# Kernel optimization log

Hardware: AMD Instinct MI355X
Metric: run time of the kernel (lower is better)

## Reference

```python
import jax, jax.numpy as jnp
import numpy as np

MIN_DIST = 4
BASE_PRIMES = np.array([2, 3, 5, 7])  # A, C, G, U
# canonical pair prime products: AU=2*7=14, CG=3*5=15, GU=5*7=35


def nussinov(s):
    """Nussinov max-score non-crossing pairing: O(N^3) DP (vectorized per
    anti-diagonal) + stack-based traceback. s: [N,N] float64, symmetric, >=0.
    Returns symmetric 0/1 pair mask. Mirrors kirigami.nussinov (CPU numpy)."""
    N = s.shape[0]
    D = np.zeros((N, N))  # D[d, i] = dp[i, i+d]
    E = np.zeros((N, N))  # E[d, j] = dp[j-d, j]
    ar = np.arange(N)
    for d in range(1, N):
        m = N - d
        pair = (D[d - 2, 1:m + 1] if d >= 2 else 0.0) + s[ar[:m], ar[:m] + d]
        # split over k=i..j-1: dp[i,k] + dp[k+1,j] (k=i covers i-unpaired)
        split = (D[0:d, 0:m] + E[d - 1::-1, d:N]).max(axis=0)
        val = np.maximum(pair, split)
        D[d, :m] = val
        E[d, d:] = val
    dp = np.zeros((N, N))
    for d in range(1, N):
        dp[ar[:N - d], ar[:N - d] + d] = D[d, :N - d]
    eps = 1e-9
    pm = np.zeros((N, N))
    stack = [(0, N - 1)]
    while stack:
        i, j = stack.pop()
        if j <= i:
            continue
        v = dp[i, j]
        if v <= eps:
            continue
        if dp[i + 1, j] >= v - eps:
            stack.append((i + 1, j))
        elif s[i, j] > 0 and dp[i + 1, j - 1] + s[i, j] >= v - eps:
            pm[i, j] = pm[j, i] = 1.0
            stack.append((i + 1, j - 1))
        else:
            ks = np.arange(i, j)
            k = int(ks[np.argmax(dp[i, ks] + dp[ks + 1, j])])
            stack.append((i, k))
            stack.append((k + 1, j))
    return pm


def _premask(con, feat):
    """Symmetrize + remove sharp angles (tril(-4)+triu(4)) + canonical-pair mask."""
    c = con[0, 0]                      # [N, N]
    c = (c + c.T) * 0.5                # Symmetrize
    N = c.shape[0]
    idx = jnp.arange(N)
    dist_ok = jnp.abs(idx[:, None] - idx[None, :]) >= MIN_DIST  # RemoveSharp
    seq = feat[0, :4, :, 0]            # [4, N] one-hot base encoding
    primes = jnp.asarray(BASE_PRIMES)[jnp.argmax(seq, axis=0)]  # [N]
    prod = primes[:, None] * primes[None, :]
    canon = (prod == 14) | (prod == 15) | (prod == 35)          # Canonicalize
    return c * (dist_ok & canon)


def setup_inputs() -> dict:
    key = jax.random.key(0)
    k1, k2 = jax.random.split(key)
    N = 1024
    con = jax.random.uniform(k1, (1, 1, N, N), dtype=jnp.float32)
    feat = jax.random.normal(k2, (1, 16, N, N), dtype=jnp.float32)
    return {"con": con, "feat": feat}


def reference(con, feat):
    c = _premask(con, feat)
    # original: GPU->CPU numpy float64 DP, then mask back on device
    mask = nussinov(np.asarray(c, dtype=np.float64))
    out = c * jnp.asarray(mask, dtype=c.dtype)
    return out.reshape(con.shape)
```

## Files before the change

### kernel.cpp

```cpp
#include <hip/hip_runtime.h>

#define NN 1024
#define BT 32
#define TT 32
#define NTILES ((TT * (TT + 1)) / 2)

__device__ __forceinline__ double gload_cc(const double* p) {
    double v;
    asm volatile("global_load_dwordx2 %0, %1, off sc0 sc1" : "=v"(v) : "v"(p));
    return v;
}
__device__ __forceinline__ void gstore_cc(double* p, double v) {
    asm volatile("global_store_dwordx2 %0, %1, off sc0 sc1" :: "v"(p), "v"(v));
}
__device__ __forceinline__ void gstore_flag(int* p, int v) {
    asm volatile("global_store_dword %0, %1, off sc0 sc1" :: "v"(p), "v"(v));
}
#define VWAIT0 asm volatile("s_waitcnt vmcnt(0)" ::: "memory")

__device__ __forceinline__ void waitflag2(const int* f, int a0, int b0, int a1, int b1) {
    const int* p0 = &f[(a0 * TT + b0) << 4];
    const int* p1 = &f[(a1 * TT + b1) << 4];
    int it = 0;
    while (true) {
        int v0, v1;
        asm volatile("global_load_dword %0, %2, off sc0 sc1\n\t"
                     "global_load_dword %1, %3, off sc0 sc1\n\t"
                     "s_waitcnt vmcnt(0)"
                     : "=&v"(v0), "=&v"(v1)
                     : "v"(p0), "v"(p1));
        if (v0 & v1) break;
        if (it < 8) __builtin_amdgcn_s_sleep(1);
        else        __builtin_amdgcn_s_sleep(15);
        ++it;
    }
    asm volatile("" ::: "memory");
}
__device__ __forceinline__ void waitflag4(const int* f, int a0, int b0, int a1, int b1,
                                          int a2, int b2, int a3, int b3) {
    const int* p0 = &f[(a0 * TT + b0) << 4];
    const int* p1 = &f[(a1 * TT + b1) << 4];
    const int* p2 = &f[(a2 * TT + b2) << 4];
    const int* p3 = &f[(a3 * TT + b3) << 4];
    int it = 0;
    while (true) {
        int v0, v1, v2, v3;
        asm volatile("global_load_dword %0, %4, off sc0 sc1\n\t"
                     "global_load_dword %1, %5, off sc0 sc1\n\t"
                     "global_load_dword %2, %6, off sc0 sc1\n\t"
                     "global_load_dword %3, %7, off sc0 sc1\n\t"
                     "s_waitcnt vmcnt(0)"
                     : "=&v"(v0), "=&v"(v1), "=&v"(v2), "=&v"(v3)
                     : "v"(p0), "v"(p1), "v"(p2), "v"(p3));
        if (v0 & v1 & v2 & v3) break;
        if (it < 8) __builtin_amdgcn_s_sleep(1);
        else        __builtin_amdgcn_s_sleep(15);
        ++it;
    }
    asm volatile("" ::: "memory");
}
__device__ __forceinline__ void waitflag2_blk(const int* f, int a0, int b0, int a1, int b1) {
    if (threadIdx.x < 64) waitflag2(f, a0, b0, a1, b1);
    __syncthreads();
}
__device__ __forceinline__ void waitflag4_blk(const int* f, int a0, int b0, int a1, int b1,
                                              int a2, int b2, int a3, int b3) {
    if (threadIdx.x < 64) waitflag4(f, a0, b0, a1, b1, a2, b2, a3, b3);
    __syncthreads();
}

__global__ void primes_kernel(const float* __restrict__ feat, int* __restrict__ primes) {
    int i = blockIdx.x * blockDim.x + threadIdx.x;
    if (i < NN) {
        float best = feat[i * NN];
        int arg = 0;
        for (int ch = 1; ch < 4; ++ch) {
            float v = feat[ch * NN * NN + i * NN];
            if (v > best) { best = v; arg = ch; }
        }
        const int P[4] = {2, 3, 5, 7};
        primes[i] = P[arg];
    }
}

__global__ void prep_kernel(const float* __restrict__ con, const int* __restrict__ primes,
                            float* __restrict__ S, double* __restrict__ R,
                            double* __restrict__ C, float* __restrict__ out,
                            int* __restrict__ flags,
                            int* __restrict__ qi, int* __restrict__ qj,
                            int* __restrict__ qready, int* __restrict__ qctl) {
    int idx = blockIdx.x * blockDim.x + threadIdx.x;
    int i = idx >> 10;
    int j = idx & (NN - 1);
    float c = (con[idx] + con[j * NN + i]) * 0.5f;
    int prod = primes[i] * primes[j];
    bool canon = (prod == 14) | (prod == 15) | (prod == 35);
    int d = i - j; if (d < 0) d = -d;
    S[idx] = (canon && d >= 4) ? c : 0.0f;
    R[idx] = 0.0;
    C[idx] = 0.0;
    out[idx] = 0.0f;
    if (idx < TT * TT * 16) flags[idx] = 0;
    if (idx < 4096) qready[idx] = (idx == 0) ? 1 : 0;
    if (idx == 0) {
        qi[0] = 0; qj[0] = NN - 1;
        qctl[0] = 0;
        qctl[16] = 1;
        qctl[32] = 1;
    }
}

__global__ __launch_bounds__(256) void nuss_tiles_kernel(double* __restrict__ R,
                                                         double* __restrict__ C,
                                                         const float* __restrict__ S,
                                                         int* __restrict__ flags) {
    __shared__ double DJJc[32][33];
    __shared__ double Vtc[32][33];
    __shared__ __attribute__((aligned(16))) double Ast[32][34];
    __shared__ __attribute__((aligned(16))) double Bst[32][34];
    __shared__ double Pld[32][33];
    __shared__ float  Sld[32][32];
    __shared__ double edgeCol[33];
    __shared__ __attribute__((aligned(16))) double Prt[3][32][6];

    int b = blockIdx.x, dd = 0;
    while (b >= TT - dd) { b -= TT - dd; ++dd; }
    const int I = b, J = b + dd;
    const int aI = I * BT, aJ = J * BT;
    const int tid = threadIdx.x;
    const int wid = tid >> 6;
    const int lane = tid & 63;
    const int r = lane >> 1;
    const int h = lane & 1;

    if (dd == 0) {
        #pragma unroll
        for (int w = 0; w < 4; ++w) {
            int idx = w * 256 + tid; int rr = idx >> 5, cc = idx & 31;
            Sld[rr][cc] = S[(aI + rr) * NN + aI + cc];
        }
        for (int idx = tid; idx < 32 * 33; idx += 256)
            ((double*)Vtc)[idx] = 0.0;
        __syncthreads();
        if (wid == 0) {
            double vrow[16];
            #pragma unroll
            for (int u = 0; u < 16; ++u) vrow[u] = 0.0;
            for (int s = 1; s <= 31; ++s) {
                int c = r + s;
                bool act = (c <= 31);
                double acc = 0.0;
                if (act) {
                    double t0 = 0.0, t1 = 0.0, t2 = 0.0, t3 = 0.0;
                    #pragma unroll
                    for (int u = 0; u < 16; u += 4) {
                        int k0 = h * 16 + u;
                        t0 = fmax(t0, vrow[u]     + Vtc[c][k0 + 1]);
                        t1 = fmax(t1, vrow[u + 1] + Vtc[c][k0 + 2]);
                        t2 = fmax(t2, vrow[u + 2] + Vtc[c][k0 + 3]);
                        t3 = fmax(t3, vrow[u + 3] + Vtc[c][k0 + 4]);
                    }
                    acc = fmax(fmax(t0, t1), fmax(t2, t3));
                }
                acc = fmax(acc, __shfl_xor(acc, 1));
                if (act) {
                    double best = fmax(acc, Vtc[c - 1][r + 1] + (double)Sld[r][c]);
                    if (h == 0) Vtc[c][r] = best;
                    #pragma unroll
                    for (int u = 0; u < 16; ++u)
                        if (h * 16 + u == c) vrow[u] = best;
                }
            }
        }
        __syncthreads();
        #pragma unroll
        for (int w = 0; w < 4; ++w) {
            int idx = w * 256 + tid; int rr = idx >> 5, cc = idx & 31;
            gstore_cc(&R[(aI + rr) * NN + aI + cc], Vtc[cc][rr]);
        }
        #pragma unroll
        for (int w = 0; w < 4; ++w) {
            int idx = w * 256 + tid; int cc = idx >> 5, rr = idx & 31;
            gstore_cc(&C[(aI + cc) * NN + aI + rr], Vtc[cc][rr]);
        }
        VWAIT0;
        __syncthreads();
        if (tid == 0) gstore_flag(&flags[(I * TT + I) << 4], 1);
        return;
    }

    const int nk = dd - 1;
    const int off = (wid & 1) * 16 + h * 8;
    waitflag2_blk(flags, I, I, J, J);

    double ra[4], rb[4];
    double ec = 0.0, ve = 0.0;
    double asl[8];
    double ar1 = 0.0;
    #pragma unroll
    for (int w = 0; w < 4; ++w) {
        int idx = w * 256 + tid; int cc = idx >> 5, mm = idx & 31;
        ra[w] = gload_cc(&C[(aJ + cc) * NN + aJ + mm]);
    }
    if (wid < 2) {
        #pragma unroll
        for (int u = 0; u < 8; ++u)
            asl[u] = gload_cc(&R[(aI + r) * NN + aI + off + u]);
    }
    if (r < 31) ar1 = gload_cc(&R[(aI + r) * NN + aI + r + 1]);
    if (wid == 0 && nk == 0) {
        if (lane < 33) ec = gload_cc(&R[(aI + lane) * NN + (aJ - 1)]);
        if (lane < 32) ve = gload_cc(&R[(aI + 32) * NN + aJ + lane]);
    }
    #pragma unroll
    for (int w = 0; w < 4; ++w) {
        int idx = w * 256 + tid; int rr = idx >> 5, cc = idx & 31;
        Sld[rr][cc] = S[(aI + rr) * NN + aJ + cc];
    }
    for (int idx = tid; idx < 32 * 33; idx += 256)
        ((double*)Vtc)[idx] = 0.0;
    VWAIT0;
    #pragma unroll
    for (int w = 0; w < 4; ++w) {
        int idx = w * 256 + tid; int cc = idx >> 5, mm = idx & 31;
        DJJc[cc][mm] = ra[w];
    }
    if (tid < 32) DJJc[tid][32] = 0.0;
    double slice8[8];
    if (wid < 2) {
        #pragma unroll
        for (int u = 0; u < 8; ++u)
            slice8[u] = (off + u > r + 1) ? asl[u] : -1.0e30;
    } else {
        #pragma unroll
        for (int u = 0; u < 8; ++u) slice8[u] = 0.0;
    }
    if (wid == 0 && nk == 0) {
        if (lane < 33) edgeCol[lane] = ec;
        if (lane < 32) Vtc[lane][32] = ve;
    }
    __syncthreads();

    double P[16];
    #pragma unroll
    for (int x = 0; x < 16; ++x) P[x] = 0.0;
    const int rg = lane >> 3, cg = lane & 7;
    const int r4 = rg * 4, c4 = cg * 4;

    auto kkloop = [&]() {
        for (int kk = wid * 8; kk < wid * 8 + 8; ++kk) {
            double2 av0 = *(const double2*)&Ast[kk][r4];
            double2 av1 = *(const double2*)&Ast[kk][r4 + 2];
            double2 bv0 = *(const double2*)&Bst[kk][c4];
            double2 bv1 = *(const double2*)&Bst[kk][c4 + 2];
            P[0]  = fmax(P[0],  av0.x + bv0.x); P[1]  = fmax(P[1],  av0.x + bv0.y);
            P[2]  = fmax(P[2],  av0.x + bv1.x); P[3]  = fmax(P[3],  av0.x + bv1.y);
            P[4]  = fmax(P[4],  av0.y + bv0.x); P[5]  = fmax(P[5],  av0.y + bv0.y);
            P[6]  = fmax(P[6],  av0.y + bv1.x); P[7]  = fmax(P[7],  av0.y + bv1.y);
            P[8]  = fmax(P[8],  av1.x + bv0.x); P[9]  = fmax(P[9],  av1.x + bv0.y);
            P[10] = fmax(P[10], av1.x + bv1.x); P[11] = fmax(P[11], av1.x + bv1.y);
            P[12] = fmax(P[12], av1.y + bv0.x); P[13] = fmax(P[13], av1.y + bv0.y);
            P[14] = fmax(P[14], av1.y + bv1.x); P[15] = fmax(P[15], av1.y + bv1.y);
        }
    };
    auto proc = [&](int t1, int t2, bool last) {
        if (t2 >= 0) waitflag4_blk(flags, I, t1, t1, J, I, t2, t2, J);
        else         waitflag2_blk(flags, I, t1, t1, J);
        if (last && wid == 0) {
            if (lane < 33) ec = gload_cc(&R[(aI + lane) * NN + (aJ - 1)]);
            if (lane < 32) ve = gload_cc(&R[(aI + 32) * NN + aJ + lane]);
        }
        int k1 = t1 * BT;
        #pragma unroll
        for (int w = 0; w < 4; ++w) {
            int idx = w * 256 + tid; int rr = idx >> 5, kk = idx & 31;
            ra[w] = gload_cc(&R[(aI + rr) * NN + k1 + kk]);
            rb[w] = gload_cc(&C[(aJ + rr) * NN + k1 + 1 + kk]);
        }
        VWAIT0;
        #pragma unroll
        for (int w = 0; w < 4; ++w) {
            int idx = w * 256 + tid; int rr = idx >> 5, kk = idx & 31;
            Ast[kk][rr] = ra[w];
            Bst[kk][rr] = rb[w];
        }
        if (last && wid == 0) {
            if (lane < 33) edgeCol[lane] = ec;
            if (lane < 32) Vtc[lane][32] = ve;
        }
        __syncthreads();
        if (t2 >= 0) {
            int k2 = t2 * BT;
            #pragma unroll
            for (int w = 0; w < 4; ++w) {
                int idx = w * 256 + tid; int rr = idx >> 5, kk = idx & 31;
                ra[w] = gload_cc(&R[(aI + rr) * NN + k2 + kk]);
                rb[w] = gload_cc(&C[(aJ + rr) * NN + k2 + 1 + kk]);
            }
        }
        kkloop();
        if (t2 >= 0) {
            __syncthreads();
            VWAIT0;
            #pragma unroll
            for (int w = 0; w < 4; ++w) {
                int idx = w * 256 + tid; int rr = idx >> 5, kk = idx & 31;
                Ast[kk][rr] = ra[w];
                Bst[kk][rr] = rb[w];
            }
            __syncthreads();
            kkloop();
        }
        __syncthreads();
    };

    {
        int tl = (I + J) >> 1, tr = ((I + J) >> 1) + 1;
        int pend = -1;
        for (int q = 0; q < nk; ++q) {
            int t;
            if ((q & 1) == 0) { if (tl >= I + 1) t = tl--; else t = tr++; }
            else              { if (tr <= J - 1) t = tr++; else t = tl--; }
            if (pend < 0) { pend = t; continue; }
            int rp = (pend - I > J - pend) ? pend - I : J - pend;
            int rt = (t - I > J - t) ? t - I : J - t;
            if (rp == rt) { proc(pend, t, q == nk - 1); pend = -1; }
            else          { proc(pend, -1, false); pend = t; }
        }
        if (pend >= 0) proc(pend, -1, true);
    }

    if (nk > 0) {
        if (wid == 0) {
            #pragma unroll
            for (int x = 0; x < 4; ++x)
                #pragma unroll
                for (int y = 0; y < 4; ++y)
                    Pld[r4 + x][c4 + y] = P[x * 4 + y];
        }
        __syncthreads();
        if (wid == 1) {
            #pragma unroll
            for (int x = 0; x < 4; ++x)
                #pragma unroll
                for (int y = 0; y < 4; ++y)
                    Pld[r4 + x][c4 + y] = fmax(Pld[r4 + x][c4 + y], P[x * 4 + y]);
        }
        __syncthreads();
        if (wid == 2) {
            #pragma unroll
            for (int x = 0; x < 4; ++x)
                #pragma unroll
                for (int y = 0; y < 4; ++y)
                    Pld[r4 + x][c4 + y] = fmax(Pld[r4 + x][c4 + y], P[x * 4 + y]);
        }
        __syncthreads();
        if (wid == 3) {
            #pragma unroll
            for (int x = 0; x < 4; ++x)
                #pragma unroll
                for (int y = 0; y < 4; ++y)
                    Pld[r4 + x][c4 + y] = fmax(Pld[r4 + x][c4 + y], P[x * 4 + y]);
        }
        __syncthreads();
    } else {
        for (int idx = tid; idx < 32 * 33; idx += 256)
            ((double*)Pld)[idx] = 0.0;
        __syncthreads();
    }

    {
        const double* bsel = (wid < 2) ? &Vtc[0][0] : &DJJc[0][0];
        double ecr = edgeCol[r];
        double ecp = edgeCol[r + 1];
        double pv[8];
        double p1 = 0.0, p2 = 0.0, shc = 0.0, shp = 0.0, erc = 0.0, erp = 0.0;

#define PREFQ(SS)                                                     \
    { int cq_ = (r + (SS) - 31) & 31;                                 \
      const double* bp_ = bsel + cq_ * 33 + off + 1;                  \
      _Pragma("unroll")                                               \
      for (int u = 0; u < 8; ++u) pv[u] = bp_[u]; }

#define PARTQ(SS)                                                     \
    { double t0_ = fmax(slice8[0] + pv[0], slice8[1] + pv[1]);        \
      double t1_ = fmax(slice8[2] + pv[2], slice8[3] + pv[3]);        \
      double t2_ = fmax(slice8[4] + pv[4], slice8[5] + pv[5]);        \
      double t3_ = fmax(slice8[6] + pv[6], slice8[7] + pv[7]);        \
      double pa_ = fmax(fmax(t0_, t1_), fmax(t2_, t3_));              \
      pa_ = fmax(pa_, __shfl_xor(pa_, 1));                            \
      if (h == 0) Prt[(SS) % 3][r][wid] = pa_; }

#define STEPB(SS)                                                     \
    { int c_ = r + (SS) - 31;                                         \
      bool act_ = ((unsigned)c_ < 32u);                               \
      int cc_ = c_ & 31;                                              \
      double a0_ = Prt[(SS) % 3][r][0];                               \
      double a1_ = Prt[(SS) % 3][r][1];                               \
      double a2_ = Prt[(SS) % 3][r][2];                               \
      double a3_ = Prt[(SS) % 3][r][3];                               \
      double er_  = Vtc[cc_][32];                                     \
      double dj0_ = DJJc[cc_][0];                                     \
      double dj1_ = DJJc[cc_][(cc_ > 0) ? cc_ - 1 : 0];               \
      double pld_ = Pld[r][cc_];                                      \
      float  sld_ = Sld[r][cc_];                                      \
      shp = shc; erp = erc; erc = er_;                                \
      shc = __shfl_down(p1, 2);                                       \
      double shd_ = __shfl_down(p2, 4);                               \
      double acc_ = fmax(fmax(a0_, a1_), fmax(a2_, a3_));             \
      if (act_) {                                                     \
          double b0_ = fmax(acc_, (r == 31) ? erc : shc);             \
          double b1_ = (r < 31) ? (ar1 + ((r == 30) ? erc : shd_))    \
                                : -1.0e30;                            \
          double b2_ = fmax(p1, p2 + dj1_);                           \
          double b3_ = fmax(ecr + dj0_, pld_);                        \
          double pv_ = (c_ == 0) ? ecp : ((r == 31) ? erp : shp);     \
          double b4_ = fmax(pv_ + (double)sld_, b1_);                 \
          double best_ = fmax(fmax(b0_, b2_), fmax(b3_, b4_));        \
          if (wid == 0 && h == 0) Vtc[c_][r] = best_;                 \
          if (wid >= 2) {                                             \
              _Pragma("unroll")                                       \
              for (int u = 0; u < 8; ++u)                             \
                  if (off + u == c_) slice8[u] = best_;               \
          }                                                           \
          p2 = p1; p1 = best_;                                        \
      } else { p2 = p1; }                                             \
      __syncthreads(); }

        PREFQ(0) PARTQ(0)
        PREFQ(1) PARTQ(1)
        __syncthreads();
        for (int s3 = 0; s3 < 63; s3 += 3) {
            PREFQ(s3 + 2) PARTQ(s3 + 2)
            STEPB(s3)
            PREFQ(s3 + 3) PARTQ(s3 + 3)
            STEPB(s3 + 1)
            PREFQ(s3 + 4) PARTQ(s3 + 4)
            STEPB(s3 + 2)
        }
#undef PREFQ
#undef PARTQ
#undef STEPB
    }
    __syncthreads();

    #pragma unroll
    for (int w = 0; w < 4; ++w) {
        int idx = w * 256 + tid; int rr = idx >> 5, cc = idx & 31;
        gstore_cc(&R[(aI + rr) * NN + aJ + cc], Vtc[cc][rr]);
    }
    #pragma unroll
    for (int w = 0; w < 4; ++w) {
        int idx = w * 256 + tid; int cc = idx >> 5, rr = idx & 31;
        gstore_cc(&C[(aJ + cc) * NN + aI + rr], Vtc[cc][rr]);
    }
    VWAIT0;
    __syncthreads();
    if (tid == 0) gstore_flag(&flags[(I * TT + J) << 4], 1);
}

__global__ __launch_bounds__(256) void traceback_kernel(const double* __restrict__ R,
                                                        const double* __restrict__ C,
                                                        const float* __restrict__ S,
                                                        float* __restrict__ out,
                                                        int* __restrict__ qi,
                                                        int* __restrict__ qj,
                                                        int* __restrict__ qready,
                                                        int* __restrict__ qctl) {
    __shared__ double Rw[16][17];
    __shared__ float  Sw[16][17];
    __shared__ int sh_cmd, sh_i, sh_j;
    __shared__ double sred_v[4];
    __shared__ int sred_k[4];
    const double eps = 1e-9;
    const int tid = threadIdx.x;
    int* headp = qctl;
    int* tailp = qctl + 16;
    int* pendp = qctl + 32;

    int i = 0, j = 0; double v = 0.0;
    bool have = false;
    int ai = -(1 << 29), aj = 0;
    int myidx = -1;

    while (true) {
        if (tid == 0) {
            int cmd;
            int guard = 0;
            while (true) {
                if (!have) {
                    if (++guard > (1 << 22)) { cmd = -1; break; }
                    if (myidx < 0) myidx = atomicAdd(headp, 1);
                    int rdy = 0;
                    if (myidx < 4096)
                        rdy = __hip_atomic_load(&qready[myidx], __ATOMIC_RELAXED,
                                                __HIP_MEMORY_SCOPE_AGENT);
                    if (rdy) {
                        int ni, nj;
                        asm volatile("global_load_dword %0, %2, off sc0 sc1\n\t"
                                     "global_load_dword %1, %3, off sc0 sc1\n\t"
                                     "s_waitcnt vmcnt(0)"
                                     : "=&v"(ni), "=&v"(nj)
                                     : "v"(&qi[myidx]), "v"(&qj[myidx]));
                        myidx = -1;
                        i = ni; j = nj;
                        if (j <= i) { atomicAdd(pendp, -1); continue; }
                        v = R[i * NN + j];
                        if (v <= eps) { atomicAdd(pendp, -1); continue; }
                        have = true;
                        continue;
                    }
                    int pend = __hip_atomic_load(pendp, __ATOMIC_RELAXED,
                                                 __HIP_MEMORY_SCOPE_AGENT);
                    if (pend == 0) { cmd = -1; break; }
                    __builtin_amdgcn_s_sleep(2);
                    continue;
                }
                int u = i - ai, w = aj - j;
                if ((unsigned)u > 15u || (unsigned)w > 14u) { cmd = 1; break; }
                double a = Rw[u][w];
                if (a >= v - eps) {
                    ++i; v = a;
                    if (j <= i || v <= eps) { have = false; atomicAdd(pendp, -1); }
                    continue;
                }
                float sv = Sw[u][w];
                double b2 = Rw[u][w + 1];
                if (sv > 0.0f && b2 + (double)sv >= v - eps) {
                    out[i * NN + j] = sv; out[j * NN + i] = sv;
                    ++i; --j; v = b2;
                    if (j <= i || v <= eps) { have = false; atomicAdd(pendp, -1); }
                    continue;
                }
                cmd = 0; break;
            }
            sh_cmd = cmd; sh_i = i; sh_j = j;
        }
        __syncthreads();
        int cmd = sh_cmd;
        if (cmd < 0) break;

        if (cmd == 1) {
            int i0 = sh_i, j0 = sh_j;
            int di = tid >> 4, dj = tid & 15;
            int rr = i0 + 1 + di; if (rr > NN - 1) rr = NN - 1;
            int cc = j0 - dj;     if (cc < 0) cc = 0;
            Rw[di][dj] = R[rr * NN + cc];
            int sr = i0 + di;     if (sr > NN - 1) sr = NN - 1;
            Sw[di][dj] = S[sr * NN + cc];
            __syncthreads();
            if (tid == 0) { ai = i0; aj = j0; }
            continue;
        }

        const int si = sh_i, sj = sh_j;
        double bv = -1.0; int bk = 0x7fffffff;
        for (int k = si + tid; k < sj; k += 256) {
            double tv = R[si * NN + k] + C[sj * NN + k + 1];
            if (tv > bv) { bv = tv; bk = k; }
        }
        for (int offr = 32; offr; offr >>= 1) {
            double ov = __shfl_down(bv, offr);
            int    ok = __shfl_down(bk, offr);
            if (ov > bv || (ov == bv && ok < bk)) { bv = ov; bk = ok; }
        }
        if ((tid & 63) == 0) { sred_v[tid >> 6] = bv; sred_k[tid >> 6] = bk; }
        __syncthreads();
        if (tid == 0) {
            double fv = sred_v[0]; int fk = sred_k[0];
            for (int w = 1; w < 4; ++w)
                if (sred_v[w] > fv || (sred_v[w] == fv && sred_k[w] < fk)) { fv = sred_v[w]; fk = sred_k[w]; }
            int slot = atomicAdd(tailp, 1);
            int rv = fk + 1;
            asm volatile("global_store_dword %0, %1, off sc0 sc1" :: "v"(&qi[slot]), "v"(rv));
            asm volatile("global_store_dword %0, %1, off sc0 sc1" :: "v"(&qj[slot]), "v"(sj));
            VWAIT0;
            atomicAdd(pendp, 1);
            VWAIT0;
            gstore_flag(&qready[slot], 1);
            j = fk;
            if (j <= i) { have = false; atomicAdd(pendp, -1); }
            else {
                v = R[i * NN + j];
                if (v <= eps) { have = false; atomicAdd(pendp, -1); }
                else have = true;
            }
        }
        __syncthreads();
    }
}

extern "C" void kernel_launch(void* const* d_in, const int* in_sizes, int n_in,
                              void* d_out, int out_size, void* d_ws, size_t ws_size,
                              hipStream_t stream) {
    const float* con  = (const float*)d_in[0];
    const float* feat = (const float*)d_in[1];
    float* out = (float*)d_out;

    char* ws = (char*)d_ws;
    double* R      = (double*)(ws);
    double* C      = (double*)(ws + (size_t)8  * 1024 * 1024);
    float*  S      = (float*) (ws + (size_t)16 * 1024 * 1024);
    int*    primes = (int*)   (ws + (size_t)20 * 1024 * 1024);
    int*    flags  = (int*)   (ws + (size_t)20 * 1024 * 1024 + 8192);
    char*   qbase  = ws + (size_t)20 * 1024 * 1024 + 128 * 1024;
    int*    qi     = (int*)(qbase);
    int*    qj     = (int*)(qbase + 16 * 1024);
    int*    qready = (int*)(qbase + 32 * 1024);
    int*    qctl   = (int*)(qbase + 48 * 1024);

    primes_kernel<<<(NN + 255) / 256, 256, 0, stream>>>(feat, primes);
    prep_kernel<<<(NN * NN) / 256, 256, 0, stream>>>(con, primes, S, R, C, out, flags,
                                                     qi, qj, qready, qctl);
    nuss_tiles_kernel<<<NTILES, 256, 0, stream>>>(R, C, S, flags);
    traceback_kernel<<<64, 256, 0, stream>>>(R, C, S, out, qi, qj, qready, qctl);
}
```

Measured before the change: 1.180 ms.

## Process two wavefront steps per barrier in the tile diagonal recurrence

Restructures the per-anti-diagonal recurrence so each barrier interval handles two serial steps instead of one. Partial maxima for two future steps are computed after the barrier into a 4-slot ring buffer. To make this legal, the k=i+1 split term now comes from registers (ar2, p3, a third shuffle, dj2), and the shared-memory partial excludes that column. This roughly halves the __syncthreads count in the latency-bound 64-step loop, at the cost of extra shuffles and registers per step.

```diff
diff --git a/kernel.cpp b/kernel.cpp
--- a/kernel.cpp
+++ b/kernel.cpp
@@ -121,7 +121,7 @@
     __shared__ double Pld[32][33];
     __shared__ float  Sld[32][32];
     __shared__ double edgeCol[33];
-    __shared__ __attribute__((aligned(16))) double Prt[3][32][6];
+    __shared__ __attribute__((aligned(16))) double Prt[4][32][6];
 
     int b = blockIdx.x, dd = 0;
     while (b >= TT - dd) { b -= TT - dd; ++dd; }
@@ -196,7 +196,7 @@
     double ra[4], rb[4];
     double ec = 0.0, ve = 0.0;
     double asl[8];
-    double ar1 = 0.0;
+    double ar1 = 0.0, ar2 = 0.0;
     #pragma unroll
     for (int w = 0; w < 4; ++w) {
         int idx = w * 256 + tid; int cc = idx >> 5, mm = idx & 31;
@@ -208,6 +208,7 @@
             asl[u] = gload_cc(&R[(aI + r) * NN + aI + off + u]);
     }
     if (r < 31) ar1 = gload_cc(&R[(aI + r) * NN + aI + r + 1]);
+    if (r < 30) ar2 = gload_cc(&R[(aI + r) * NN + aI + r + 2]);
     if (wid == 0 && nk == 0) {
         if (lane < 33) ec = gload_cc(&R[(aI + lane) * NN + (aJ - 1)]);
         if (lane < 32) ve = gload_cc(&R[(aI + 32) * NN + aJ + lane]);
@@ -230,7 +231,7 @@
     if (wid < 2) {
         #pragma unroll
         for (int u = 0; u < 8; ++u)
-            slice8[u] = (off + u > r + 1) ? asl[u] : -1.0e30;
+            slice8[u] = (off + u > r + 2) ? asl[u] : -1.0e30;
     } else {
         #pragma unroll
         for (int u = 0; u < 8; ++u) slice8[u] = 0.0;
@@ -374,7 +375,8 @@
         double ecr = edgeCol[r];
         double ecp = edgeCol[r + 1];
         double pv[8];
-        double p1 = 0.0, p2 = 0.0, shc = 0.0, shp = 0.0, erc = 0.0, erp = 0.0;
+        double p1 = 0.0, p2 = 0.0, p3 = 0.0;
+        double shc = 0.0, shp = 0.0, erc = 0.0, erp = 0.0;
 
 #define PREFQ(SS)                                                     \
     { int cq_ = (r + (SS) - 31) & 31;                                 \
@@ -389,58 +391,63 @@
       double t3_ = fmax(slice8[6] + pv[6], slice8[7] + pv[7]);        \
       double pa_ = fmax(fmax(t0_, t1_), fmax(t2_, t3_));              \
       pa_ = fmax(pa_, __shfl_xor(pa_, 1));                            \
-      if (h == 0) Prt[(SS) % 3][r][wid] = pa_; }
-
-#define STEPB(SS)                                                     \
+      if (h == 0) Prt[(SS) & 3][r][wid] = pa_; }
+
+#define TAILB(SS)                                                     \
     { int c_ = r + (SS) - 31;                                         \
       bool act_ = ((unsigned)c_ < 32u);                               \
       int cc_ = c_ & 31;                                              \
-      double a0_ = Prt[(SS) % 3][r][0];                               \
-      double a1_ = Prt[(SS) % 3][r][1];                               \
-      double a2_ = Prt[(SS) % 3][r][2];                               \
-      double a3_ = Prt[(SS) % 3][r][3];                               \
+      double a0_ = Prt[(SS) & 3][r][0];                               \
+      double a1_ = Prt[(SS) & 3][r][1];                               \
+      double a2_ = Prt[(SS) & 3][r][2];                               \
+      double a3_ = Prt[(SS) & 3][r][3];                               \
       double er_  = Vtc[cc_][32];                                     \
       double dj0_ = DJJc[cc_][0];                                     \
       double dj1_ = DJJc[cc_][(cc_ > 0) ? cc_ - 1 : 0];               \
+      double dj2_ = DJJc[cc_][(cc_ > 1) ? cc_ - 2 : 0];               \
       double pld_ = Pld[r][cc_];                                      \
       float  sld_ = Sld[r][cc_];                                      \
       shp = shc; erp = erc; erc = er_;                                \
       shc = __shfl_down(p1, 2);                                       \
       double shd_ = __shfl_down(p2, 4);                               \
+      double she_ = __shfl_down(p3, 6);                               \
       double acc_ = fmax(fmax(a0_, a1_), fmax(a2_, a3_));             \
       if (act_) {                                                     \
           double b0_ = fmax(acc_, (r == 31) ? erc : shc);             \
           double b1_ = (r < 31) ? (ar1 + ((r == 30) ? erc : shd_))    \
                                 : -1.0e30;                            \
+          double b5_ = (r < 30) ? (ar2 + ((r == 29) ? erc : she_))    \
+                                : -1.0e30;                            \
           double b2_ = fmax(p1, p2 + dj1_);                           \
+          double b6_ = p3 + dj2_;                                     \
           double b3_ = fmax(ecr + dj0_, pld_);                        \
-          double pv_ = (c_ == 0) ? ecp : ((r == 31) ? erp : shp);     \
-          double b4_ = fmax(pv_ + (double)sld_, b1_);                 \
-          double best_ = fmax(fmax(b0_, b2_), fmax(b3_, b4_));        \
+          double pvv_ = (c_ == 0) ? ecp : ((r == 31) ? erp : shp);    \
+          double b4_ = fmax(pvv_ + (double)sld_, fmax(b1_, b5_));     \
+          double best_ = fmax(fmax(b0_, fmax(b2_, b6_)),              \
+                              fmax(b3_, b4_));                        \
           if (wid == 0 && h == 0) Vtc[c_][r] = best_;                 \
           if (wid >= 2) {                                             \
               _Pragma("unroll")                                       \
               for (int u = 0; u < 8; ++u)                             \
                   if (off + u == c_) slice8[u] = best_;               \
           }                                                           \
-          p2 = p1; p1 = best_;                                        \
-      } else { p2 = p1; }                                             \
-      __syncthreads(); }
+          p3 = p2; p2 = p1; p1 = best_;                               \
+      } else { p3 = p2; p2 = p1; }                                    \
+    }
 
         PREFQ(0) PARTQ(0)
         PREFQ(1) PARTQ(1)
         __syncthreads();
-        for (int s3 = 0; s3 < 63; s3 += 3) {
-            PREFQ(s3 + 2) PARTQ(s3 + 2)
-            STEPB(s3)
-            PREFQ(s3 + 3) PARTQ(s3 + 3)
-            STEPB(s3 + 1)
-            PREFQ(s3 + 4) PARTQ(s3 + 4)
-            STEPB(s3 + 2)
+        for (int s2 = 0; s2 < 64; s2 += 2) {
+            TAILB(s2)
+            TAILB(s2 + 1)
+            PREFQ(s2 + 2) PARTQ(s2 + 2)
+            PREFQ(s2 + 3) PARTQ(s2 + 3)
+            __syncthreads();
         }
 #undef PREFQ
 #undef PARTQ
-#undef STEPB
+#undef TAILB
     }
     __syncthreads();
 
```

Measured after the change: 1.209 ms. 1.02x slower.
